# Kernel tuning notes

Measured on AMD Instinct MI355X. Metric: run time of the kernel, lower is better.

## Reference

```python
import jax, jax.numpy as jnp
import numpy as np
import math

B, H, S, DK = 4, 16, 2048, 64

def setup_inputs() -> dict:
    key = jax.random.key(0)
    kq, kk, kv, km = jax.random.split(key, 4)
    Q = jax.random.normal(kq, (B, H, S, DK), dtype=jnp.float32)
    K = jax.random.normal(kk, (B, H, S, DK), dtype=jnp.float32)
    V = jax.random.normal(kv, (B, H, S, DK), dtype=jnp.float32)
    # boolean mask [B, Sq, Sk]; True positions are masked out (set to -1e9)
    mask = jax.random.randint(km, (B, S, S), 0, 2).astype(jnp.bool_)
    return {"Q": Q, "K": K, "V": V, "mask": mask}

def reference(Q, K, V, mask):
    d_k = Q.shape[-1]
    # [B,H,Sq,Sk] scores
    scores = jnp.einsum('bhqd,bhkd->bhqk', Q, K) / math.sqrt(d_k)
    # mask [B,Sq,Sk] broadcasts over head dim (torch code repeats over heads)
    scores = jnp.where(mask[:, None, :, :], jnp.float32(-1e9), scores)
    attn = jax.nn.softmax(scores, axis=-1)
    out = jnp.einsum('bhqk,bhkd->bhqd', attn, V)
    return (out, attn)
```

## Files before the change

kernel.cpp:

```cpp
#include <hip/hip_runtime.h>
#include <cstdint>
#include <cstddef>

#define S_LEN 2048
#define DKD   64
#define BQ    64
#define BK    128
#define NKT   16
#define BDIM  256

typedef float f32x4 __attribute__((ext_vector_type(4)));
typedef short s16x8 __attribute__((ext_vector_type(8)));
typedef short s16x4 __attribute__((ext_vector_type(4)));
typedef unsigned short u16t;
typedef unsigned long long u64t;

#define KS_OFF    0
#define KT_BYTES  (BK * DKD * 2)
#define VT_OFF    16384
#define VT_BYTES  (DKD * BK * 2)
#define PS_OFF    32768
#define PS_STRIDE 264
#define SMEM_SZ   (PS_OFF + BQ * PS_STRIDE)

__device__ __forceinline__ u16t f2bf(float f) {
  unsigned u = __builtin_bit_cast(unsigned, f);
  return (u16t)((u + 0x7FFFu + ((u >> 16) & 1u)) >> 16);
}

__device__ __forceinline__ void gl_lds16(const void* g, void* l) {
  typedef __attribute__((address_space(1))) void gvoid;
  typedef __attribute__((address_space(3))) void lvoid;
  __builtin_amdgcn_global_load_lds((gvoid*)(void*)g, (lvoid*)l, 16, 0, 0);
}

__global__ __launch_bounds__(256)
void pack_mask(const unsigned char* __restrict__ Mg, u64t* __restrict__ bits) {
  __shared__ int mflag_s;
  const int tid = threadIdx.x;
  int f = 0;
  for (int i = tid; i < 4096; i += 256) if ((i & 3) && Mg[i]) f = 1;
  if (tid == 0) mflag_s = 0;
  __syncthreads();
  if (f) mflag_s = 1;
  __syncthreads();
  const int mstride = mflag_s ? 1 : 4;

  const int row = blockIdx.x * 8 + (tid >> 5);
  const int wd  = tid & 31;
  const size_t kbase = (size_t)row * S_LEN + (size_t)wd * 64;
  u64t word = 0;
  if (mstride == 1) {
    const u64t* p = (const u64t*)(Mg + kbase);
    #pragma unroll
    for (int i = 0; i < 8; ++i) {
      u64t x = p[i];
      u64t nz = x | (x >> 4); nz |= nz >> 2; nz |= nz >> 1;
      nz &= 0x0101010101010101ull;
      word |= ((nz * 0x0102040810204080ull) >> 56) << (8 * i);
    }
  } else {
    const unsigned* p = (const unsigned*)Mg + kbase;
    #pragma unroll
    for (int i = 0; i < 64; ++i) word |= (u64t)(p[i] ? 1u : 0u) << i;
  }
  bits[(size_t)row * 32 + wd] = word;
}

__global__ __launch_bounds__(256)
void conv_k(const float* __restrict__ Kg, u16t* __restrict__ Kws) {
  const int tid = threadIdx.x;
  const int bh = blockIdx.x >> 4, kt = blockIdx.x & 15;
  const float* src = Kg + ((size_t)bh * S_LEN + (size_t)kt * BK) * DKD;
  u16t* dst = Kws + (size_t)blockIdx.x * (BK * DKD);
  #pragma unroll
  for (int i = 0; i < 4; ++i) {
    int c = tid + 256 * i;
    int row = c >> 3, y = c & 7;
    int oc = y ^ (row & 7);
    const float4* s4 = (const float4*)(src + row * DKD + 8 * oc);
    float4 a = s4[0], b = s4[1];
    s16x8 h = { (short)f2bf(a.x), (short)f2bf(a.y), (short)f2bf(a.z), (short)f2bf(a.w),
                (short)f2bf(b.x), (short)f2bf(b.y), (short)f2bf(b.z), (short)f2bf(b.w) };
    *(s16x8*)(dst + row * DKD + 8 * y) = h;
  }
}

__global__ __launch_bounds__(256)
void conv_v(const float* __restrict__ Vg, u16t* __restrict__ Vws) {
  __shared__ float scr[BK][DKD + 1];
  const int tid = threadIdx.x;
  const float4* src = (const float4*)(Vg + (size_t)blockIdx.x * (BK * DKD));
  #pragma unroll
  for (int i = 0; i < 8; ++i) {
    int c = tid + 256 * i;
    float4 v = src[c];
    int k = c >> 4, d0 = (c & 15) * 4;
    scr[k][d0] = v.x; scr[k][d0 + 1] = v.y; scr[k][d0 + 2] = v.z; scr[k][d0 + 3] = v.w;
  }
  __syncthreads();
  u16t* dst = Vws + (size_t)blockIdx.x * (DKD * BK);
  #pragma unroll
  for (int i = 0; i < 8; ++i) {
    int c = tid + 256 * i;
    int dv = c >> 5, y = c & 31;
    int k0 = 4 * (y ^ (dv & 7));
    ushort4 h = make_ushort4(f2bf(scr[k0][dv]), f2bf(scr[k0 + 1][dv]),
                             f2bf(scr[k0 + 2][dv]), f2bf(scr[k0 + 3][dv]));
    *(ushort4*)(dst + dv * BK + 4 * y) = h;
  }
}

__global__ __launch_bounds__(256)
void attn_ws(const float* __restrict__ Qg, const u16t* __restrict__ Kws,
             const u16t* __restrict__ Vws, const u64t* __restrict__ bits,
             float* __restrict__ outg, float* __restrict__ attng) {
  __shared__ char smem[SMEM_SZ];
  const int tid = threadIdx.x;
  const int p = blockIdx.x;
  const int qb = (p >> 3) & 31;
  const int bh = (p & 7) + 8 * (p >> 8);
  const int b  = bh >> 4;
  const int lane = tid & 63, wv = tid >> 6;
  const int cl = lane & 15, g = lane >> 4;
  const int q0 = qb * BQ + 16 * wv + 4 * g;
  const int swzK = (cl & 7) << 4;
  const int swzV = (cl & 7) << 3;

  const char* Kbh = (const char*)Kws + (size_t)bh * NKT * KT_BYTES;
  const char* Vbh = (const char*)Vws + (size_t)bh * NKT * VT_BYTES;

  float* aRow[4]; float* oRow[4]; const u64t* bitRow[4];
  #pragma unroll
  for (int r = 0; r < 4; ++r) {
    aRow[r] = attng + (size_t)(bh * S_LEN + q0 + r) * S_LEN + cl;
    oRow[r] = outg  + (size_t)(bh * S_LEN + q0 + r) * DKD + cl;
    bitRow[r] = bits + (size_t)(b * S_LEN + q0 + r) * 32;
  }

  s16x8 aq0, aq1;
  {
    const float* qrow = Qg + ((size_t)bh * S_LEN + qb * BQ + 16 * wv + cl) * DKD;
    float x[8], y[8];
    *(float4*)(x)     = *(const float4*)(qrow + 8 * g);
    *(float4*)(x + 4) = *(const float4*)(qrow + 8 * g + 4);
    *(float4*)(y)     = *(const float4*)(qrow + 32 + 8 * g);
    *(float4*)(y + 4) = *(const float4*)(qrow + 32 + 8 * g + 4);
    #pragma unroll
    for (int j = 0; j < 8; ++j) { aq0[j] = (short)f2bf(x[j]); aq1[j] = (short)f2bf(y[j]); }
  }

  auto stageK = [&](int kt) {
    const char* src = Kbh + (size_t)kt * KT_BYTES + wv * 4096 + lane * 16;
    #pragma unroll
    for (int t = 0; t < 4; ++t)
      gl_lds16(src + t * 1024, (void*)(smem + KS_OFF + wv * 4096 + t * 1024));
  };
  auto stageV = [&](int kt) {
    const char* src = Vbh + (size_t)kt * VT_BYTES + wv * 4096 + lane * 16;
    #pragma unroll
    for (int t = 0; t < 4; ++t)
      gl_lds16(src + t * 1024, (void*)(smem + VT_OFF + wv * 4096 + t * 1024));
  };

  float lsum[4] = {0.f, 0.f, 0.f, 0.f};
  for (int kt = 0; kt < NKT; ++kt) {
    stageK(kt);
    __syncthreads();
    f32x4 accs[8];
    #pragma unroll
    for (int s = 0; s < 8; ++s) {
      const char* rb = smem + KS_OFF + (16 * s + cl) * 128;
      s16x8 b0 = *(const s16x8*)(rb + ((16 * g) ^ swzK));
      s16x8 b1 = *(const s16x8*)(rb + ((64 + 16 * g) ^ swzK));
      f32x4 acc = {0.f, 0.f, 0.f, 0.f};
      acc = __builtin_amdgcn_mfma_f32_16x16x32_bf16(aq0, b0, acc, 0, 0, 0);
      acc = __builtin_amdgcn_mfma_f32_16x16x32_bf16(aq1, b1, acc, 0, 0, 0);
      accs[s] = acc;
    }
    u64t bw0[4], bw1[4];
    #pragma unroll
    for (int r = 0; r < 4; ++r) { bw0[r] = bitRow[r][2 * kt]; bw1[r] = bitRow[r][2 * kt + 1]; }
    #pragma unroll
    for (int r = 0; r < 4; ++r) {
      float sum = 0.f;
      #pragma unroll
      for (int s = 0; s < 8; ++s) {
        bool mk = (((s < 4) ? bw0[r] : bw1[r]) >> ((16 * s + cl) & 63)) & 1ull;
        float e = __expf(accs[s][r] * 0.125f);
        sum += mk ? 0.f : e;
      }
      lsum[r] += sum;
    }
    __syncthreads();
  }
  float rinv[4];
  #pragma unroll
  for (int r = 0; r < 4; ++r) {
    float l = lsum[r];
    #pragma unroll
    for (int d = 1; d < 16; d <<= 1) l += __shfl_xor(l, d);
    rinv[r] = 1.f / l;
  }

  f32x4 accpv[4];
  #pragma unroll
  for (int db = 0; db < 4; ++db) accpv[db] = (f32x4){0.f, 0.f, 0.f, 0.f};

  for (int kt = 0; kt < NKT; ++kt) {
    stageK(kt);
    stageV(kt);
    __syncthreads();
    u64t bw0[4], bw1[4];
    #pragma unroll
    for (int r = 0; r < 4; ++r) { bw0[r] = bitRow[r][2 * kt]; bw1[r] = bitRow[r][2 * kt + 1]; }

    #pragma unroll
    for (int ks = 0; ks < 4; ++ks) {
      f32x4 qa[2];
      #pragma unroll
      for (int sp = 0; sp < 2; ++sp) {
        int s = 2 * ks + sp;
        const char* rb = smem + KS_OFF + (16 * s + cl) * 128;
        s16x8 b0 = *(const s16x8*)(rb + ((16 * g) ^ swzK));
        s16x8 b1 = *(const s16x8*)(rb + ((64 + 16 * g) ^ swzK));
        f32x4 acc = {0.f, 0.f, 0.f, 0.f};
        acc = __builtin_amdgcn_mfma_f32_16x16x32_bf16(aq0, b0, acc, 0, 0, 0);
        acc = __builtin_amdgcn_mfma_f32_16x16x32_bf16(aq1, b1, acc, 0, 0, 0);
        qa[sp] = acc;
      }
      #pragma unroll
      for (int sp = 0; sp < 2; ++sp) {
        int s = 2 * ks + sp;
        #pragma unroll
        for (int r = 0; r < 4; ++r) {
          bool mk = (((s < 4) ? bw0[r] : bw1[r]) >> ((16 * s + cl) & 63)) & 1ull;
          float pv = mk ? 0.f : __expf(qa[sp][r] * 0.125f) * rinv[r];
          __builtin_nontemporal_store(pv, aRow[r] + kt * BK + 16 * s);
          *(u16t*)(smem + PS_OFF + (16 * wv + 4 * g + r) * PS_STRIDE +
                   (32 * ks + 16 * sp + cl) * 2) = f2bf(pv);
        }
      }
      s16x4 p0 = *(const s16x4*)(smem + PS_OFF + (16 * wv + cl) * PS_STRIDE + (32 * ks + 4 * g) * 2);
      s16x4 p1 = *(const s16x4*)(smem + PS_OFF + (16 * wv + cl) * PS_STRIDE + (32 * ks + 16 + 4 * g) * 2);
      s16x8 pa = __builtin_shufflevector(p0, p1, 0, 1, 2, 3, 4, 5, 6, 7);
      #pragma unroll
      for (int db = 0; db < 4; ++db) {
        const char* vrow = smem + VT_OFF + (16 * db + cl) * 256;
        s16x4 v0 = *(const s16x4*)(vrow + ((64 * ks + 8 * g) ^ swzV));
        s16x4 v1 = *(const s16x4*)(vrow + ((64 * ks + 32 + 8 * g) ^ swzV));
        s16x8 vb = __builtin_shufflevector(v0, v1, 0, 1, 2, 3, 4, 5, 6, 7);
        accpv[db] = __builtin_amdgcn_mfma_f32_16x16x32_bf16(pa, vb, accpv[db], 0, 0, 0);
      }
    }
    __syncthreads();
  }

  #pragma unroll
  for (int db = 0; db < 4; ++db)
    #pragma unroll
    for (int r = 0; r < 4; ++r)
      oRow[r][16 * db] = accpv[db][r];
}

#define FB_KSTR 144
#define FB_VOFF (BK * FB_KSTR)
#define FB_VSTR 272
#define FB_POFF (FB_VOFF + DKD * FB_VSTR)
#define FB_SMEM (FB_POFF + BQ * FB_VSTR)

__global__ __launch_bounds__(256)
void attn_fb(const float* __restrict__ Qg, const float* __restrict__ Kg,
             const float* __restrict__ Vg, const unsigned char* __restrict__ Mg,
             float* __restrict__ outg, float* __restrict__ attng) {
  __shared__ char smem[FB_SMEM];
  __shared__ int mflag_s;
  const int tid = threadIdx.x;
  const int p = blockIdx.x;
  const int qb = (p >> 3) & 31;
  const int bh = (p & 7) + 8 * (p >> 8);
  const int b  = bh >> 4;

  int f = 0;
  for (int i = tid; i < 4096; i += BDIM) if ((i & 3) && Mg[i]) f = 1;
  if (tid == 0) mflag_s = 0;
  __syncthreads();
  if (f) mflag_s = 1;
  __syncthreads();
  const int mstride = mflag_s ? 1 : 4;

  const int lane = tid & 63, wv = tid >> 6;
  const int cl = lane & 15, g = lane >> 4;
  const int q0 = qb * BQ + 16 * wv + 4 * g;

  const float* Kbh = Kg + (size_t)bh * S_LEN * DKD;
  const float* Vbh = Vg + (size_t)bh * S_LEN * DKD;

  float* aRow[4]; float* oRow[4]; const unsigned char* mRow[4];
  #pragma unroll
  for (int r = 0; r < 4; ++r) {
    aRow[r] = attng + (size_t)(bh * S_LEN + q0 + r) * S_LEN + cl;
    oRow[r] = outg + (size_t)(bh * S_LEN + q0 + r) * DKD + cl;
    mRow[r] = Mg + ((size_t)(b * S_LEN + q0 + r) * S_LEN + cl) * (size_t)mstride;
  }

  s16x8 aq0, aq1;
  {
    const float* qrow = Qg + ((size_t)bh * S_LEN + qb * BQ + 16 * wv + cl) * DKD;
    float x[8], y[8];
    *(float4*)(x)     = *(const float4*)(qrow + 8 * g);
    *(float4*)(x + 4) = *(const float4*)(qrow + 8 * g + 4);
    *(float4*)(y)     = *(const float4*)(qrow + 32 + 8 * g);
    *(float4*)(y + 4) = *(const float4*)(qrow + 32 + 8 * g + 4);
    #pragma unroll
    for (int j = 0; j < 8; ++j) { aq0[j] = (short)f2bf(x[j]); aq1[j] = (short)f2bf(y[j]); }
  }

  float lsum[4] = {0.f, 0.f, 0.f, 0.f};
  for (int kt = 0; kt < NKT; ++kt) {
    const float4* ksrc = (const float4*)(Kbh + (size_t)kt * (BK * DKD));
    #pragma unroll
    for (int it = 0; it < 8; ++it) {
      int c = tid + BDIM * it;
      float4 v = ksrc[c];
      *(ushort4*)(smem + (c >> 4) * FB_KSTR + (c & 15) * 8) =
          make_ushort4(f2bf(v.x), f2bf(v.y), f2bf(v.z), f2bf(v.w));
    }
    __syncthreads();
    #pragma unroll
    for (int s = 0; s < 8; ++s) {
      s16x8 b0 = *(const s16x8*)(smem + (16 * s + cl) * FB_KSTR + 16 * g);
      s16x8 b1 = *(const s16x8*)(smem + (16 * s + cl) * FB_KSTR + 64 + 16 * g);
      f32x4 acc = {0.f, 0.f, 0.f, 0.f};
      acc = __builtin_amdgcn_mfma_f32_16x16x32_bf16(aq0, b0, acc, 0, 0, 0);
      acc = __builtin_amdgcn_mfma_f32_16x16x32_bf16(aq1, b1, acc, 0, 0, 0);
      #pragma unroll
      for (int r = 0; r < 4; ++r) {
        bool mk = mRow[r][(size_t)(kt * BK + 16 * s) * mstride] != 0;
        lsum[r] += mk ? 0.f : __expf(acc[r] * 0.125f);
      }
    }
    __syncthreads();
  }
  float rinv[4];
  #pragma unroll
  for (int r = 0; r < 4; ++r) {
    float l = lsum[r];
    #pragma unroll
    for (int d = 1; d < 16; d <<= 1) l += __shfl_xor(l, d);
    rinv[r] = 1.f / l;
  }

  f32x4 accpv[4];
  #pragma unroll
  for (int db = 0; db < 4; ++db) accpv[db] = (f32x4){0.f, 0.f, 0.f, 0.f};

  for (int kt = 0; kt < NKT; ++kt) {
    const float4* ksrc = (const float4*)(Kbh + (size_t)kt * (BK * DKD));
    #pragma unroll
    for (int it = 0; it < 8; ++it) {
      int c = tid + BDIM * it;
      float4 v = ksrc[c];
      *(ushort4*)(smem + (c >> 4) * FB_KSTR + (c & 15) * 8) =
          make_ushort4(f2bf(v.x), f2bf(v.y), f2bf(v.z), f2bf(v.w));
    }
    const float4* vsrc = (const float4*)(Vbh + (size_t)kt * (BK * DKD));
    #pragma unroll
    for (int it = 0; it < 8; ++it) {
      int c = tid + BDIM * it;
      float4 v = vsrc[c];
      int k = c >> 4, d0 = (c & 15) * 4;
      *(u16t*)(smem + FB_VOFF + (d0 + 0) * FB_VSTR + k * 2) = f2bf(v.x);
      *(u16t*)(smem + FB_VOFF + (d0 + 1) * FB_VSTR + k * 2) = f2bf(v.y);
      *(u16t*)(smem + FB_VOFF + (d0 + 2) * FB_VSTR + k * 2) = f2bf(v.z);
      *(u16t*)(smem + FB_VOFF + (d0 + 3) * FB_VSTR + k * 2) = f2bf(v.w);
    }
    __syncthreads();

    #pragma unroll
    for (int ks = 0; ks < 4; ++ks) {
      f32x4 qa[2];
      #pragma unroll
      for (int sp = 0; sp < 2; ++sp) {
        int s = 2 * ks + sp;
        s16x8 b0 = *(const s16x8*)(smem + (16 * s + cl) * FB_KSTR + 16 * g);
        s16x8 b1 = *(const s16x8*)(smem + (16 * s + cl) * FB_KSTR + 64 + 16 * g);
        f32x4 acc = {0.f, 0.f, 0.f, 0.f};
        acc = __builtin_amdgcn_mfma_f32_16x16x32_bf16(aq0, b0, acc, 0, 0, 0);
        acc = __builtin_amdgcn_mfma_f32_16x16x32_bf16(aq1, b1, acc, 0, 0, 0);
        qa[sp] = acc;
      }
      #pragma unroll
      for (int sp = 0; sp < 2; ++sp) {
        int s = 2 * ks + sp;
        #pragma unroll
        for (int r = 0; r < 4; ++r) {
          bool mk = mRow[r][(size_t)(kt * BK + 16 * s) * mstride] != 0;
          float pv = mk ? 0.f : __expf(qa[sp][r] * 0.125f) * rinv[r];
          __builtin_nontemporal_store(pv, aRow[r] + kt * BK + 16 * s);
          *(u16t*)(smem + FB_POFF + (16 * wv + 4 * g + r) * FB_VSTR +
                   (32 * ks + 16 * sp + cl) * 2) = f2bf(pv);
        }
      }
      s16x4 p0 = *(const s16x4*)(smem + FB_POFF + (16 * wv + cl) * FB_VSTR + (32 * ks + 4 * g) * 2);
      s16x4 p1 = *(const s16x4*)(smem + FB_POFF + (16 * wv + cl) * FB_VSTR + (32 * ks + 16 + 4 * g) * 2);
      s16x8 pa = __builtin_shufflevector(p0, p1, 0, 1, 2, 3, 4, 5, 6, 7);
      #pragma unroll
      for (int db = 0; db < 4; ++db) {
        s16x4 v0 = *(const s16x4*)(smem + FB_VOFF + (16 * db + cl) * FB_VSTR + (32 * ks + 4 * g) * 2);
        s16x4 v1 = *(const s16x4*)(smem + FB_VOFF + (16 * db + cl) * FB_VSTR + (32 * ks + 16 + 4 * g) * 2);
        s16x8 vb = __builtin_shufflevector(v0, v1, 0, 1, 2, 3, 4, 5, 6, 7);
        accpv[db] = __builtin_amdgcn_mfma_f32_16x16x32_bf16(pa, vb, accpv[db], 0, 0, 0);
      }
    }
    __syncthreads();
  }

  #pragma unroll
  for (int db = 0; db < 4; ++db)
    #pragma unroll
    for (int r = 0; r < 4; ++r)
      oRow[r][16 * db] = accpv[db][r];
}

extern "C" void kernel_launch(void* const* d_in, const int* in_sizes, int n_in,
                              void* d_out, int out_size, void* d_ws, size_t ws_size,
                              hipStream_t stream) {
  const float* Q = (const float*)d_in[0];
  const float* K = (const float*)d_in[1];
  const float* V = (const float*)d_in[2];
  const unsigned char* M = (const unsigned char*)d_in[3];
  float* out = (float*)d_out;
  float* attn = out + (size_t)4 * 16 * S_LEN * DKD;

  const size_t BITS_SZ = (size_t)4 * S_LEN * 32 * 8;
  const size_t KWS_SZ  = (size_t)64 * NKT * BK * DKD * 2;
  const size_t VWS_SZ  = (size_t)64 * NKT * DKD * BK * 2;
  if (ws_size >= BITS_SZ + KWS_SZ + VWS_SZ) {
    u64t* bits = (u64t*)d_ws;
    u16t* Kws = (u16t*)((char*)d_ws + BITS_SZ);
    u16t* Vws = (u16t*)((char*)d_ws + BITS_SZ + KWS_SZ);
    pack_mask<<<1024, 256, 0, stream>>>(M, bits);
    conv_k<<<1024, 256, 0, stream>>>(K, Kws);
    conv_v<<<1024, 256, 0, stream>>>(V, Vws);
    attn_ws<<<2048, BDIM, 0, stream>>>(Q, Kws, Vws, bits, out, attn);
  } else {
    attn_fb<<<2048, BDIM, 0, stream>>>(Q, K, V, M, out, attn);
  }
}
```

Baseline: 366.0 us.

## Vectorize attention-probability stores from LDS, prefetch K/V tiles, merge prologue kernels

The per-element scalar nontemporal stores of the attention matrix are replaced with a cooperative pass that reads the bf16 probability tile from LDS and writes 16-byte vectorized rows. This targets the large attn write, which dominates memory traffic. The first pass now double-buffers K tiles using custom waitcnt/barrier macros, and the second pass prefetches the next K/V tile after the barrier. The three preprocessing kernels are merged into one launch. Stored attention probabilities now come from bf16-rounded values rather than fp32, which lowers the precision of that output.

Result: no change. 367.5 us (+0.4%).

```diff
diff --git a/kernel.cpp b/kernel.cpp
--- a/kernel.cpp
+++ b/kernel.cpp
@@ -27,6 +27,12 @@
   unsigned u = __builtin_bit_cast(unsigned, f);
   return (u16t)((u + 0x7FFFu + ((u >> 16) & 1u)) >> 16);
 }
+__device__ __forceinline__ float bf_lo(unsigned u) {
+  return __builtin_bit_cast(float, u << 16);
+}
+__device__ __forceinline__ float bf_hi(unsigned u) {
+  return __builtin_bit_cast(float, u & 0xFFFF0000u);
+}
 
 __device__ __forceinline__ void gl_lds16(const void* g, void* l) {
   typedef __attribute__((address_space(1))) void gvoid;
@@ -34,80 +40,84 @@
   __builtin_amdgcn_global_load_lds((gvoid*)(void*)g, (lvoid*)l, 16, 0, 0);
 }
 
+#define BAR_VM(N) do { asm volatile("s_waitcnt vmcnt(" #N ")\n\ts_barrier" ::: "memory"); \
+                       __builtin_amdgcn_sched_barrier(0); } while (0)
+#define BAR_LGKM() do { asm volatile("s_waitcnt lgkmcnt(0)\n\ts_barrier" ::: "memory"); \
+                        __builtin_amdgcn_sched_barrier(0); } while (0)
+
 __global__ __launch_bounds__(256)
-void pack_mask(const unsigned char* __restrict__ Mg, u64t* __restrict__ bits) {
+void prologue(const unsigned char* __restrict__ Mg, const float* __restrict__ Kg,
+              const float* __restrict__ Vg, u64t* __restrict__ bits,
+              u16t* __restrict__ Kws, u16t* __restrict__ Vws) {
+  __shared__ float scr[BK][DKD + 1];
   __shared__ int mflag_s;
   const int tid = threadIdx.x;
-  int f = 0;
-  for (int i = tid; i < 4096; i += 256) if ((i & 3) && Mg[i]) f = 1;
-  if (tid == 0) mflag_s = 0;
-  __syncthreads();
-  if (f) mflag_s = 1;
-  __syncthreads();
-  const int mstride = mflag_s ? 1 : 4;
-
-  const int row = blockIdx.x * 8 + (tid >> 5);
-  const int wd  = tid & 31;
-  const size_t kbase = (size_t)row * S_LEN + (size_t)wd * 64;
-  u64t word = 0;
-  if (mstride == 1) {
-    const u64t* p = (const u64t*)(Mg + kbase);
+  const int bid = blockIdx.x;
+
+  if (bid < 1024) {
+    int f = 0;
+    for (int i = tid; i < 4096; i += 256) if ((i & 3) && Mg[i]) f = 1;
+    if (tid == 0) mflag_s = 0;
+    __syncthreads();
+    if (f) mflag_s = 1;
+    __syncthreads();
+    const int mstride = mflag_s ? 1 : 4;
+
+    const int row = bid * 8 + (tid >> 5);
+    const int wd  = tid & 31;
+    const size_t kbase = (size_t)row * S_LEN + (size_t)wd * 64;
+    u64t word = 0;
+    if (mstride == 1) {
+      const u64t* p = (const u64t*)(Mg + kbase);
+      #pragma unroll
+      for (int i = 0; i < 8; ++i) {
+        u64t x = p[i];
+        u64t nz = x | (x >> 4); nz |= nz >> 2; nz |= nz >> 1;
+        nz &= 0x0101010101010101ull;
+        word |= ((nz * 0x0102040810204080ull) >> 56) << (8 * i);
+      }
+    } else {
+      const unsigned* p = (const unsigned*)Mg + kbase;
+      #pragma unroll
+      for (int i = 0; i < 64; ++i) word |= (u64t)(p[i] ? 1u : 0u) << i;
+    }
+    bits[(size_t)row * 32 + wd] = word;
+  } else if (bid < 2048) {
+    const int kb = bid - 1024;
+    const float* src = Kg + (size_t)kb * (BK * DKD);
+    u16t* dst = Kws + (size_t)kb * (BK * DKD);
+    #pragma unroll
+    for (int i = 0; i < 4; ++i) {
+      int c = tid + 256 * i;
+      int row = c >> 3, y = c & 7;
+      int oc = y ^ (row & 7);
+      const float4* s4 = (const float4*)(src + row * DKD + 8 * oc);
+      float4 a = s4[0], b = s4[1];
+      s16x8 h = { (short)f2bf(a.x), (short)f2bf(a.y), (short)f2bf(a.z), (short)f2bf(a.w),
+                  (short)f2bf(b.x), (short)f2bf(b.y), (short)f2bf(b.z), (short)f2bf(b.w) };
+      *(s16x8*)(dst + row * DKD + 8 * y) = h;
+    }
+  } else {
+    const int vb = bid - 2048;
+    const float4* src = (const float4*)(Vg + (size_t)vb * (BK * DKD));
     #pragma unroll
     for (int i = 0; i < 8; ++i) {
-      u64t x = p[i];
-      u64t nz = x | (x >> 4); nz |= nz >> 2; nz |= nz >> 1;
-      nz &= 0x0101010101010101ull;
-      word |= ((nz * 0x0102040810204080ull) >> 56) << (8 * i);
-    }
-  } else {
-    const unsigned* p = (const unsigned*)Mg + kbase;
-    #pragma unroll
-    for (int i = 0; i < 64; ++i) word |= (u64t)(p[i] ? 1u : 0u) << i;
-  }
-  bits[(size_t)row * 32 + wd] = word;
-}
-
-__global__ __launch_bounds__(256)
-void conv_k(const float* __restrict__ Kg, u16t* __restrict__ Kws) {
-  const int tid = threadIdx.x;
-  const int bh = blockIdx.x >> 4, kt = blockIdx.x & 15;
-  const float* src = Kg + ((size_t)bh * S_LEN + (size_t)kt * BK) * DKD;
-  u16t* dst = Kws + (size_t)blockIdx.x * (BK * DKD);
-  #pragma unroll
-  for (int i = 0; i < 4; ++i) {
-    int c = tid + 256 * i;
-    int row = c >> 3, y = c & 7;
-    int oc = y ^ (row & 7);
-    const float4* s4 = (const float4*)(src + row * DKD + 8 * oc);
-    float4 a = s4[0], b = s4[1];
-    s16x8 h = { (short)f2bf(a.x), (short)f2bf(a.y), (short)f2bf(a.z), (short)f2bf(a.w),
-                (short)f2bf(b.x), (short)f2bf(b.y), (short)f2bf(b.z), (short)f2bf(b.w) };
-    *(s16x8*)(dst + row * DKD + 8 * y) = h;
-  }
-}
-
-__global__ __launch_bounds__(256)
-void conv_v(const float* __restrict__ Vg, u16t* __restrict__ Vws) {
-  __shared__ float scr[BK][DKD + 1];
-  const int tid = threadIdx.x;
-  const float4* src = (const float4*)(Vg + (size_t)blockIdx.x * (BK * DKD));
-  #pragma unroll
-  for (int i = 0; i < 8; ++i) {
-    int c = tid + 256 * i;
-    float4 v = src[c];
-    int k = c >> 4, d0 = (c & 15) * 4;
-    scr[k][d0] = v.x; scr[k][d0 + 1] = v.y; scr[k][d0 + 2] = v.z; scr[k][d0 + 3] = v.w;
-  }
-  __syncthreads();
-  u16t* dst = Vws + (size_t)blockIdx.x * (DKD * BK);
-  #pragma unroll
-  for (int i = 0; i < 8; ++i) {
-    int c = tid + 256 * i;
-    int dv = c >> 5, y = c & 31;
-    int k0 = 4 * (y ^ (dv & 7));
-    ushort4 h = make_ushort4(f2bf(scr[k0][dv]), f2bf(scr[k0 + 1][dv]),
-                             f2bf(scr[k0 + 2][dv]), f2bf(scr[k0 + 3][dv]));
-    *(ushort4*)(dst + dv * BK + 4 * y) = h;
+      int c = tid + 256 * i;
+      float4 v = src[c];
+      int k = c >> 4, d0 = (c & 15) * 4;
+      scr[k][d0] = v.x; scr[k][d0 + 1] = v.y; scr[k][d0 + 2] = v.z; scr[k][d0 + 3] = v.w;
+    }
+    __syncthreads();
+    u16t* dst = Vws + (size_t)vb * (DKD * BK);
+    #pragma unroll
+    for (int i = 0; i < 8; ++i) {
+      int c = tid + 256 * i;
+      int dv = c >> 5, y = c & 31;
+      int k0 = 4 * (y ^ (dv & 7));
+      ushort4 h = make_ushort4(f2bf(scr[k0][dv]), f2bf(scr[k0 + 1][dv]),
+                               f2bf(scr[k0 + 2][dv]), f2bf(scr[k0 + 3][dv]));
+      *(ushort4*)(dst + dv * BK + 4 * y) = h;
+    }
   }
 }
 
@@ -130,13 +140,13 @@
   const char* Kbh = (const char*)Kws + (size_t)bh * NKT * KT_BYTES;
   const char* Vbh = (const char*)Vws + (size_t)bh * NKT * VT_BYTES;
 
-  float* aRow[4]; float* oRow[4]; const u64t* bitRow[4];
+  float* oRow[4]; const u64t* bitRow[4];
   #pragma unroll
   for (int r = 0; r < 4; ++r) {
-    aRow[r] = attng + (size_t)(bh * S_LEN + q0 + r) * S_LEN + cl;
-    oRow[r] = outg  + (size_t)(bh * S_LEN + q0 + r) * DKD + cl;
+    oRow[r] = outg + (size_t)(bh * S_LEN + q0 + r) * DKD + cl;
     bitRow[r] = bits + (size_t)(b * S_LEN + q0 + r) * 32;
   }
+  float* attnQ = attng + ((size_t)bh * S_LEN + (size_t)qb * BQ) * S_LEN;
 
   s16x8 aq0, aq1;
   {
@@ -150,11 +160,11 @@
     for (int j = 0; j < 8; ++j) { aq0[j] = (short)f2bf(x[j]); aq1[j] = (short)f2bf(y[j]); }
   }
 
-  auto stageK = [&](int kt) {
+  auto stageK = [&](int kt, int off) {
     const char* src = Kbh + (size_t)kt * KT_BYTES + wv * 4096 + lane * 16;
     #pragma unroll
     for (int t = 0; t < 4; ++t)
-      gl_lds16(src + t * 1024, (void*)(smem + KS_OFF + wv * 4096 + t * 1024));
+      gl_lds16(src + t * 1024, (void*)(smem + off + wv * 4096 + t * 1024));
   };
   auto stageV = [&](int kt) {
     const char* src = Vbh + (size_t)kt * VT_BYTES + wv * 4096 + lane * 16;
@@ -164,13 +174,19 @@
   };
 
   float lsum[4] = {0.f, 0.f, 0.f, 0.f};
+  stageK(0, KS_OFF);
   for (int kt = 0; kt < NKT; ++kt) {
-    stageK(kt);
-    __syncthreads();
+    const int cur = (kt & 1) ? VT_OFF : KS_OFF;
+    if (kt + 1 < NKT) {
+      stageK(kt + 1, (kt & 1) ? KS_OFF : VT_OFF);
+      BAR_VM(4);
+    } else {
+      BAR_VM(0);
+    }
     f32x4 accs[8];
     #pragma unroll
     for (int s = 0; s < 8; ++s) {
-      const char* rb = smem + KS_OFF + (16 * s + cl) * 128;
+      const char* rb = smem + cur + (16 * s + cl) * 128;
       s16x8 b0 = *(const s16x8*)(rb + ((16 * g) ^ swzK));
       s16x8 b1 = *(const s16x8*)(rb + ((64 + 16 * g) ^ swzK));
       f32x4 acc = {0.f, 0.f, 0.f, 0.f};
@@ -192,7 +208,7 @@
       }
       lsum[r] += sum;
     }
-    __syncthreads();
+    BAR_LGKM();
   }
   float rinv[4];
   #pragma unroll
@@ -207,9 +223,9 @@
   #pragma unroll
   for (int db = 0; db < 4; ++db) accpv[db] = (f32x4){0.f, 0.f, 0.f, 0.f};
 
+  stageK(0, KS_OFF);
+  stageV(0);
   for (int kt = 0; kt < NKT; ++kt) {
-    stageK(kt);
-    stageV(kt);
     __syncthreads();
     u64t bw0[4], bw1[4];
     #pragma unroll
@@ -236,7 +252,6 @@
         for (int r = 0; r < 4; ++r) {
           bool mk = (((s < 4) ? bw0[r] : bw1[r]) >> ((16 * s + cl) & 63)) & 1ull;
           float pv = mk ? 0.f : __expf(qa[sp][r] * 0.125f) * rinv[r];
-          __builtin_nontemporal_store(pv, aRow[r] + kt * BK + 16 * s);
           *(u16t*)(smem + PS_OFF + (16 * wv + 4 * g + r) * PS_STRIDE +
                    (32 * ks + 16 * sp + cl) * 2) = f2bf(pv);
         }
@@ -254,6 +269,20 @@
       }
     }
     __syncthreads();
+
+    if (kt + 1 < NKT) { stageK(kt + 1, KS_OFF); stageV(kt + 1); }
+
+    #pragma unroll
+    for (int i = 0; i < 4; ++i) {
+      int c = tid + 256 * i;
+      int q = c >> 4, ch = c & 15;
+      uint4 d = *(const uint4*)(smem + PS_OFF + q * PS_STRIDE + ch * 16);
+      f32x4 lo = { bf_lo(d.x), bf_hi(d.x), bf_lo(d.y), bf_hi(d.y) };
+      f32x4 hi = { bf_lo(d.z), bf_hi(d.z), bf_lo(d.w), bf_hi(d.w) };
+      float* dst = attnQ + (size_t)q * S_LEN + kt * BK + ch * 8;
+      __builtin_nontemporal_store(lo, (f32x4*)dst);
+      __builtin_nontemporal_store(hi, (f32x4*)(dst + 4));
+    }
   }
 
   #pragma unroll
@@ -440,9 +469,7 @@
     u64t* bits = (u64t*)d_ws;
     u16t* Kws = (u16t*)((char*)d_ws + BITS_SZ);
     u16t* Vws = (u16t*)((char*)d_ws + BITS_SZ + KWS_SZ);
-    pack_mask<<<1024, 256, 0, stream>>>(M, bits);
-    conv_k<<<1024, 256, 0, stream>>>(K, Kws);
-    conv_v<<<1024, 256, 0, stream>>>(V, Vws);
+    prologue<<<3072, 256, 0, stream>>>(M, K, V, bits, Kws, Vws);
     attn_ws<<<2048, BDIM, 0, stream>>>(Q, Kws, Vws, bits, out, attn);
   } else {
     attn_fb<<<2048, BDIM, 0, stream>>>(Q, K, V, M, out, attn);
```
